# Optimization experiments

Hardware: AMD Instinct MI355X
Metric: run time of the kernel (lower is better)

## Reference

```python
import jax, jax.numpy as jnp
import numpy as np

D_MODEL = 1024
NUM_HEADS = 16
D_K = D_MODEL // NUM_HEADS


def setup_inputs() -> dict:
    key = jax.random.key(0)
    ks = jax.random.split(key, 8)
    B, S = 2, 2048
    query = jax.random.normal(ks[0], (B, S, D_MODEL), dtype=jnp.float32)
    k_in = jax.random.normal(ks[1], (B, S, D_MODEL), dtype=jnp.float32)
    value = jax.random.normal(ks[2], (B, S, D_MODEL), dtype=jnp.float32)
    # causal mask: True = masked out (upper triangle above diagonal)
    mask = jnp.triu(jnp.ones((S, S), dtype=bool), k=1)[None, None, :, :]
    scale = 1.0 / np.sqrt(D_MODEL)
    W_q = jax.random.normal(ks[3], (D_MODEL, D_MODEL), dtype=jnp.float32) * scale
    W_k = jax.random.normal(ks[4], (D_MODEL, D_MODEL), dtype=jnp.float32) * scale
    W_v = jax.random.normal(ks[5], (D_MODEL, D_MODEL), dtype=jnp.float32) * scale
    W_o = jax.random.normal(ks[6], (D_MODEL, D_MODEL), dtype=jnp.float32) * scale
    return {"query": query, "key": k_in, "value": value, "mask": mask,
            "W_q": W_q, "W_k": W_k, "W_v": W_v, "W_o": W_o}


def _split(x):
    # [B, S, d_model] -> [B, h, S, d_k]
    B, S, _ = x.shape
    return x.reshape(B, S, NUM_HEADS, D_K).transpose(0, 2, 1, 3)


def reference(query, key, value, mask, W_q, W_k, W_v, W_o):
    # torch nn.Linear(bias=False): y = x @ W.T
    Q = _split(query @ W_q.T)   # [B, h, Sq, d_k]
    K = _split(key @ W_k.T)     # [B, h, Sk, d_k]
    V = _split(value @ W_v.T)   # [B, h, Sk, d_k]
    scores = jnp.einsum('bhqd,bhkd->bhqk', Q, K) / jnp.sqrt(jnp.float32(D_K))
    scores = jnp.where(mask, -jnp.inf, scores)
    attn_w = jax.nn.softmax(scores, axis=-1)
    attn_w = jnp.nan_to_num(attn_w, nan=0.0)
    out = jnp.einsum('bhqk,bhkd->bhqd', attn_w, V)  # [B, h, Sq, d_k]
    B, _, Sq, _ = out.shape
    merged = out.transpose(0, 2, 1, 3).reshape(B, Sq, D_MODEL)
    return merged @ W_o.T
```

## Files before the change

### kernel.cpp

```cpp
#include <hip/hip_runtime.h>
#include <hip/hip_bf16.h>
#include <stdint.h>

typedef __attribute__((ext_vector_type(4))) float f32x4;
typedef __attribute__((ext_vector_type(8))) __bf16 bf16x8;
typedef __attribute__((ext_vector_type(4))) unsigned short us4;
typedef __attribute__((ext_vector_type(8))) unsigned short us8;

#define SEQ 2048
#define DMODEL 1024
#define NH 16
#define DK 64
#define MTOT 4096

__device__ __forceinline__ unsigned short f2bf(float x) {
  union { float f; unsigned int u; } v; v.f = x;
  unsigned int r = v.u + 0x7fffu + ((v.u >> 16) & 1u);
  return (unsigned short)(r >> 16);
}

__device__ __forceinline__ unsigned int cvtpk(float lo, float hi) {
  unsigned int r;
  asm("v_cvt_pk_bf16_f32 %0, %1, %2" : "=v"(r) : "v"(lo), "v"(hi));
  return r;
}

__device__ __forceinline__ f32x4 mfma_bf16(bf16x8 a, bf16x8 b, f32x4 c) {
  return __builtin_amdgcn_mfma_f32_16x16x32_bf16(a, b, c, 0, 0, 0);
}

__device__ __forceinline__ void gload16(const unsigned short* g, unsigned short* l) {
  __builtin_amdgcn_global_load_lds((__attribute__((address_space(1))) void*)g,
                                   (__attribute__((address_space(3))) void*)l,
                                   16, 0, 0);
}

__global__ void cvt_w(const float* __restrict__ s0, const float* __restrict__ s1,
                      const float* __restrict__ s2, const float* __restrict__ s3,
                      unsigned short* __restrict__ d0, unsigned short* __restrict__ d1,
                      unsigned short* __restrict__ d2, unsigned short* __restrict__ d3) {
  const int y = blockIdx.y;
  const float* s = y == 0 ? s0 : y == 1 ? s1 : y == 2 ? s2 : s3;
  unsigned short* d = y == 0 ? d0 : y == 1 ? d1 : y == 2 ? d2 : d3;
  const int n4 = DMODEL * DMODEL / 4;
  const int stride = gridDim.x * blockDim.x;
  for (int i = blockIdx.x * blockDim.x + threadIdx.x; i < n4; i += stride) {
    f32x4 v = reinterpret_cast<const f32x4*>(s)[i];
    us4 o;
    o.x = f2bf(v.x); o.y = f2bf(v.y); o.z = f2bf(v.z); o.w = f2bf(v.w);
    reinterpret_cast<us4*>(d)[i] = o;
  }
}

__global__ __launch_bounds__(256) void gemm_qk(
    const float* __restrict__ xq, const float* __restrict__ xk,
    const unsigned short* __restrict__ bwq, const unsigned short* __restrict__ bwk,
    unsigned short* __restrict__ Qh, unsigned short* __restrict__ Kh) {
  const int z = blockIdx.z;
  const float* A = z ? xk : xq;
  const unsigned short* B = z ? bwk : bwq;
  unsigned short* out = z ? Kh : Qh;
  const float scale = z ? 1.0f : 0.18033688011112042f;

  __shared__ __align__(16) unsigned short lA[128 * 32];
  __shared__ __align__(16) unsigned short lB[128 * 32];
  const int tid = threadIdx.x;
  const int lane = tid & 63;
  const int wid = tid >> 6;
  const int l15 = lane & 15, l4 = lane >> 4;
  const int bm = blockIdx.x, bn = blockIdx.y;
  const int wr = wid >> 1, wc = wid & 1;

  f32x4 acc[4][4] = {};

  const int chunk0 = (wid * 2 + 0) * 64 + lane;
  const int chunk1 = (wid * 2 + 1) * 64 + lane;
  const float* gAf0 = A + (size_t)(bm * 128 + (chunk0 >> 2)) * 1024 + (chunk0 & 3) * 8;
  const float* gAf1 = A + (size_t)(bm * 128 + (chunk1 >> 2)) * 1024 + (chunk1 & 3) * 8;
  const unsigned short* gB0 = B + (size_t)(bn * 128 + (chunk0 >> 2)) * 1024 + (chunk0 & 3) * 8;
  const unsigned short* gB1 = B + (size_t)(bn * 128 + (chunk1 >> 2)) * 1024 + (chunk1 & 3) * 8;
  unsigned short* wA0 = lA + chunk0 * 8;
  unsigned short* wA1 = lA + chunk1 * 8;
  unsigned short* lB0 = lB + (wid * 2 + 0) * 512;
  unsigned short* lB1 = lB + (wid * 2 + 1) * 512;

  f32x4 ra0 = *reinterpret_cast<const f32x4*>(gAf0);
  f32x4 ra1 = *reinterpret_cast<const f32x4*>(gAf0 + 4);
  f32x4 rb0 = *reinterpret_cast<const f32x4*>(gAf1);
  f32x4 rb1 = *reinterpret_cast<const f32x4*>(gAf1 + 4);

  for (int kt = 0; kt < 1024; kt += 32) {
    __syncthreads();
    union { us8 h; unsigned int u[4]; } p0, p1;
    p0.u[0] = cvtpk(ra0.x, ra0.y); p0.u[1] = cvtpk(ra0.z, ra0.w);
    p0.u[2] = cvtpk(ra1.x, ra1.y); p0.u[3] = cvtpk(ra1.z, ra1.w);
    p1.u[0] = cvtpk(rb0.x, rb0.y); p1.u[1] = cvtpk(rb0.z, rb0.w);
    p1.u[2] = cvtpk(rb1.x, rb1.y); p1.u[3] = cvtpk(rb1.z, rb1.w);
    *reinterpret_cast<us8*>(wA0) = p0.h;
    *reinterpret_cast<us8*>(wA1) = p1.h;
    gload16(gB0 + kt, lB0);
    gload16(gB1 + kt, lB1);
    if (kt + 32 < 1024) {
      ra0 = *reinterpret_cast<const f32x4*>(gAf0 + kt + 32);
      ra1 = *reinterpret_cast<const f32x4*>(gAf0 + kt + 36);
      rb0 = *reinterpret_cast<const f32x4*>(gAf1 + kt + 32);
      rb1 = *reinterpret_cast<const f32x4*>(gAf1 + kt + 36);
    }
    __syncthreads();
    bf16x8 af[4], bfr[4];
#pragma unroll
    for (int i = 0; i < 4; ++i)
      af[i] = *reinterpret_cast<const bf16x8*>(&lA[(wr * 64 + i * 16 + l15) * 32 + l4 * 8]);
#pragma unroll
    for (int j = 0; j < 4; ++j)
      bfr[j] = *reinterpret_cast<const bf16x8*>(&lB[(wc * 64 + j * 16 + l15) * 32 + l4 * 8]);
#pragma unroll
    for (int i = 0; i < 4; ++i)
#pragma unroll
      for (int j = 0; j < 4; ++j)
        acc[i][j] = mfma_bf16(bfr[j], af[i], acc[i][j]);
  }

  const int row0 = bm * 128 + wr * 64;
  const int col0 = bn * 128 + wc * 64;
#pragma unroll
  for (int i = 0; i < 4; ++i) {
    const int m = row0 + i * 16 + l15;
    const int b = m >> 11, s = m & 2047;
#pragma unroll
    for (int j = 0; j < 4; ++j) {
      const int n0 = col0 + j * 16 + l4 * 4;
      const int h = n0 >> 6, dd = n0 & 63;
      union { us4 h4; unsigned int u[2]; } pk;
      pk.u[0] = cvtpk(acc[i][j][0] * scale, acc[i][j][1] * scale);
      pk.u[1] = cvtpk(acc[i][j][2] * scale, acc[i][j][3] * scale);
      *reinterpret_cast<us4*>(&out[(size_t)(b * NH + h) * (SEQ * DK) + s * DK + dd]) = pk.h4;
    }
  }
}

__global__ __launch_bounds__(256) void gemm_v(
    const float* __restrict__ xv, const unsigned short* __restrict__ bwv,
    unsigned short* __restrict__ Vt) {
  __shared__ __align__(16) unsigned short lA[128 * 32];
  __shared__ __align__(16) unsigned short lB[128 * 32];
  const int tid = threadIdx.x;
  const int lane = tid & 63;
  const int wid = tid >> 6;
  const int l15 = lane & 15, l4 = lane >> 4;
  const int bm = blockIdx.x, bn = blockIdx.y;
  const int wr = wid >> 1, wc = wid & 1;

  f32x4 acc[4][4] = {};

  const int chunk0 = (wid * 2 + 0) * 64 + lane;
  const int chunk1 = (wid * 2 + 1) * 64 + lane;
  const float* gAf0 = xv + (size_t)(bm * 128 + (chunk0 >> 2)) * 1024 + (chunk0 & 3) * 8;
  const float* gAf1 = xv + (size_t)(bm * 128 + (chunk1 >> 2)) * 1024 + (chunk1 & 3) * 8;
  const unsigned short* gB0 = bwv + (size_t)(bn * 128 + (chunk0 >> 2)) * 1024 + (chunk0 & 3) * 8;
  const unsigned short* gB1 = bwv + (size_t)(bn * 128 + (chunk1 >> 2)) * 1024 + (chunk1 & 3) * 8;
  unsigned short* wA0 = lA + chunk0 * 8;
  unsigned short* wA1 = lA + chunk1 * 8;
  unsigned short* lB0 = lB + (wid * 2 + 0) * 512;
  unsigned short* lB1 = lB + (wid * 2 + 1) * 512;

  f32x4 ra0 = *reinterpret_cast<const f32x4*>(gAf0);
  f32x4 ra1 = *reinterpret_cast<const f32x4*>(gAf0 + 4);
  f32x4 rb0 = *reinterpret_cast<const f32x4*>(gAf1);
  f32x4 rb1 = *reinterpret_cast<const f32x4*>(gAf1 + 4);

  for (int kt = 0; kt < 1024; kt += 32) {
    __syncthreads();
    union { us8 h; unsigned int u[4]; } p0, p1;
    p0.u[0] = cvtpk(ra0.x, ra0.y); p0.u[1] = cvtpk(ra0.z, ra0.w);
    p0.u[2] = cvtpk(ra1.x, ra1.y); p0.u[3] = cvtpk(ra1.z, ra1.w);
    p1.u[0] = cvtpk(rb0.x, rb0.y); p1.u[1] = cvtpk(rb0.z, rb0.w);
    p1.u[2] = cvtpk(rb1.x, rb1.y); p1.u[3] = cvtpk(rb1.z, rb1.w);
    *reinterpret_cast<us8*>(wA0) = p0.h;
    *reinterpret_cast<us8*>(wA1) = p1.h;
    gload16(gB0 + kt, lB0);
    gload16(gB1 + kt, lB1);
    if (kt + 32 < 1024) {
      ra0 = *reinterpret_cast<const f32x4*>(gAf0 + kt + 32);
      ra1 = *reinterpret_cast<const f32x4*>(gAf0 + kt + 36);
      rb0 = *reinterpret_cast<const f32x4*>(gAf1 + kt + 32);
      rb1 = *reinterpret_cast<const f32x4*>(gAf1 + kt + 36);
    }
    __syncthreads();
    bf16x8 af[4], bfr[4];
#pragma unroll
    for (int i = 0; i < 4; ++i)
      af[i] = *reinterpret_cast<const bf16x8*>(&lA[(wr * 64 + i * 16 + l15) * 32 + l4 * 8]);
#pragma unroll
    for (int j = 0; j < 4; ++j)
      bfr[j] = *reinterpret_cast<const bf16x8*>(&lB[(wc * 64 + j * 16 + l15) * 32 + l4 * 8]);
#pragma unroll
    for (int i = 0; i < 4; ++i)
#pragma unroll
      for (int j = 0; j < 4; ++j)
        acc[i][j] = mfma_bf16(af[i], bfr[j], acc[i][j]);
  }

  const int row0 = bm * 128 + wr * 64;
  const int col0 = bn * 128 + wc * 64;
#pragma unroll
  for (int i = 0; i < 4; ++i) {
    const int m0 = row0 + i * 16 + l4 * 4;
    const int b = m0 >> 11, s0 = m0 & 2047;
    const int g = (s0 >> 2) & 7;
    const int col = (s0 & ~31) + ((g & 3) << 3) + ((g >> 2) << 2);
#pragma unroll
    for (int j = 0; j < 4; ++j) {
      const int n = col0 + j * 16 + l15;
      const int h = n >> 6, dd = n & 63;
      union { us4 h4; unsigned int u[2]; } pk;
      pk.u[0] = cvtpk(acc[i][j][0], acc[i][j][1]);
      pk.u[1] = cvtpk(acc[i][j][2], acc[i][j][3]);
      *reinterpret_cast<us4*>(&Vt[(size_t)(b * NH + h) * (DK * SEQ) + dd * SEQ + col]) = pk.h4;
    }
  }
}

__global__ __launch_bounds__(256) void gemm_o(const unsigned short* __restrict__ A,
                                              const unsigned short* __restrict__ B,
                                              float* __restrict__ out) {
  __shared__ __align__(16) unsigned short lA[128 * 32];
  __shared__ __align__(16) unsigned short lB[128 * 32];
  const int tid = threadIdx.x;
  const int lane = tid & 63;
  const int wid = tid >> 6;
  const int l15 = lane & 15, l4 = lane >> 4;
  const int bm = blockIdx.x, bn = blockIdx.y;
  const int wr = wid >> 1, wc = wid & 1;

  f32x4 acc[4][4] = {};

  const int chunk0 = (wid * 2 + 0) * 64 + lane;
  const int chunk1 = (wid * 2 + 1) * 64 + lane;
  const unsigned short* gA0 = A + (size_t)(bm * 128 + (chunk0 >> 2)) * 1024 + (chunk0 & 3) * 8;
  const unsigned short* gA1 = A + (size_t)(bm * 128 + (chunk1 >> 2)) * 1024 + (chunk1 & 3) * 8;
  const unsigned short* gB0 = B + (size_t)(bn * 128 + (chunk0 >> 2)) * 1024 + (chunk0 & 3) * 8;
  const unsigned short* gB1 = B + (size_t)(bn * 128 + (chunk1 >> 2)) * 1024 + (chunk1 & 3) * 8;
  unsigned short* lA0 = lA + (wid * 2 + 0) * 512;
  unsigned short* lA1 = lA + (wid * 2 + 1) * 512;
  unsigned short* lB0 = lB + (wid * 2 + 0) * 512;
  unsigned short* lB1 = lB + (wid * 2 + 1) * 512;

  for (int kt = 0; kt < 1024; kt += 32) {
    __syncthreads();
    gload16(gA0 + kt, lA0);
    gload16(gA1 + kt, lA1);
    gload16(gB0 + kt, lB0);
    gload16(gB1 + kt, lB1);
    __syncthreads();
    bf16x8 af[4], bfr[4];
#pragma unroll
    for (int i = 0; i < 4; ++i)
      af[i] = *reinterpret_cast<const bf16x8*>(&lA[(wr * 64 + i * 16 + l15) * 32 + l4 * 8]);
#pragma unroll
    for (int j = 0; j < 4; ++j)
      bfr[j] = *reinterpret_cast<const bf16x8*>(&lB[(wc * 64 + j * 16 + l15) * 32 + l4 * 8]);
#pragma unroll
    for (int i = 0; i < 4; ++i)
#pragma unroll
      for (int j = 0; j < 4; ++j)
        acc[i][j] = mfma_bf16(bfr[j], af[i], acc[i][j]);
  }

  const int row0 = bm * 128 + wr * 64;
  const int col0 = bn * 128 + wc * 64;
#pragma unroll
  for (int i = 0; i < 4; ++i) {
    const int m = row0 + i * 16 + l15;
#pragma unroll
    for (int j = 0; j < 4; ++j) {
      const int n0 = col0 + j * 16 + l4 * 4;
      *reinterpret_cast<f32x4*>(&out[(size_t)m * DMODEL + n0]) = acc[i][j];
    }
  }
}

__global__ __launch_bounds__(512, 2) void attn_kernel(const unsigned short* __restrict__ Qh,
                                                      const unsigned short* __restrict__ Kh,
                                                      const unsigned short* __restrict__ Vt,
                                                      unsigned short* __restrict__ Mg) {
  __shared__ __align__(16) unsigned short Kl[4][64 * 64];
  __shared__ __align__(16) unsigned short Vl[4][64 * 64];

  const int tid = threadIdx.x;
  const int lane = tid & 63;
  const int w = tid >> 6;
  const int l15 = lane & 15, l4 = lane >> 4;

  const int d = blockIdx.x;
  const int xcd = d & 7;
  const int j = d >> 3;
  const int bh = (j >> 3) * 8 + xcd;
  const int x = j & 7;

  const unsigned short* Qb = Qh + (size_t)bh * SEQ * DK;
  const unsigned short* Kb = Kh + (size_t)bh * SEQ * DK;
  const unsigned short* Vb = Vt + (size_t)bh * DK * SEQ;
  const int bq = bh >> 4, hh = bh & 15;
  unsigned short* Mbase = Mg + (size_t)bq * SEQ * DMODEL + hh * DK;

  const int srow = lane >> 3;
  const int sswz = (lane & 7) ^ srow;
  const unsigned short* KsrcB = Kb + (size_t)(w * 8 + srow) * DK + sswz * 8;
  const unsigned short* VsrcB = Vb + (size_t)(w * 8 + srow) * SEQ + sswz * 8;

  const int l7 = l15 & 7;

  const int taus[2] = {15 - x, x};

#pragma unroll 1
  for (int seg = 0; seg < 2; ++seg) {
    const int tau = taus[seg];
    const int qbase = tau * 128;
    const int q0w = qbase + w * 16;
    const int nt = 2 * tau + 2;

    __syncthreads();

    bf16x8 qf0 = *reinterpret_cast<const bf16x8*>(Qb + (size_t)(q0w + l15) * DK + l4 * 8);
    bf16x8 qf1 = *reinterpret_cast<const bf16x8*>(Qb + (size_t)(q0w + l15) * DK + 32 + l4 * 8);

    f32x4 o[4] = {};
    float mrow = -__builtin_inff();
    float lrow = 0.0f;

    gload16(KsrcB, &Kl[0][w * 512]);
    gload16(VsrcB, &Vl[0][w * 512]);
    gload16(KsrcB + (size_t)64 * DK, &Kl[1][w * 512]);
    gload16(VsrcB + 64, &Vl[1][w * 512]);

    const int S = nt >> 1;
#pragma unroll 1
    for (int s = 0; s < S; ++s) {
      const int t0 = s << 1;
      const int kbase0 = t0 << 6;

      asm volatile("s_waitcnt vmcnt(0)" ::: "memory");
      __builtin_amdgcn_sched_barrier(0);
      __builtin_amdgcn_s_barrier();
      __builtin_amdgcn_sched_barrier(0);

      if (t0 + 2 < nt) {
        gload16(KsrcB + (size_t)(kbase0 + 128) * DK, &Kl[(t0 + 2) & 3][w * 512]);
        gload16(VsrcB + (kbase0 + 128), &Vl[(t0 + 2) & 3][w * 512]);
        gload16(KsrcB + (size_t)(kbase0 + 192) * DK, &Kl[(t0 + 3) & 3][w * 512]);
        gload16(VsrcB + (kbase0 + 192), &Vl[(t0 + 3) & 3][w * 512]);
      }

#pragma unroll
      for (int u = 0; u < 2; ++u) {
        const int t = t0 + u;
        const int kbase = t << 6;
        if (kbase >= q0w + 16) continue;
        const unsigned short* Kc = Kl[t & 3];
        const unsigned short* Vc = Vl[t & 3];

        f32x4 sc[4];
        __builtin_amdgcn_s_setprio(1);
#pragma unroll
        for (int c = 0; c < 4; ++c) {
          const int krow = c * 16 + l15;
          bf16x8 kf0 = *reinterpret_cast<const bf16x8*>(&Kc[krow * 64 + ((l4 ^ l7) * 8)]);
          bf16x8 kf1 = *reinterpret_cast<const bf16x8*>(&Kc[krow * 64 + (((4 + l4) ^ l7) * 8)]);
          f32x4 z = {0.f, 0.f, 0.f, 0.f};
          z = mfma_bf16(kf0, qf0, z);
          sc[c] = mfma_bf16(kf1, qf1, z);
        }
        __builtin_amdgcn_s_setprio(0);

        if (kbase + 63 > q0w) {
          const int qg = q0w + l15;
#pragma unroll
          for (int c = 0; c < 4; ++c) {
            const int kp = kbase + c * 16 + l4 * 4;
#pragma unroll
            for (int r = 0; r < 4; ++r)
              if (kp + r > qg) sc[c][r] = -__builtin_inff();
          }
        }

        f32x4 mv = sc[0];
#pragma unroll
        for (int c = 1; c < 4; ++c)
#pragma unroll
          for (int r = 0; r < 4; ++r) mv[r] = fmaxf(mv[r], sc[c][r]);
        float pm = fmaxf(fmaxf(mv[0], mv[1]), fmaxf(mv[2], mv[3]));
        if (!__all(pm - mrow <= 8.0f)) {
          pm = fmaxf(pm, __shfl_xor(pm, 16));
          pm = fmaxf(pm, __shfl_xor(pm, 32));
          const float mn = fmaxf(mrow, pm);
          const float al = __builtin_amdgcn_exp2f(mrow - mn);
          mrow = mn;
          lrow *= al;
#pragma unroll
          for (int dd = 0; dd < 4; ++dd)
#pragma unroll
            for (int r = 0; r < 4; ++r) o[dd][r] *= al;
        }
        union PB { bf16x8 v; unsigned int u[4]; } pbv[2];
        f32x4 sv = {0.f, 0.f, 0.f, 0.f};
#pragma unroll
        for (int c = 0; c < 4; ++c) {
          const float p0 = __builtin_amdgcn_exp2f(sc[c][0] - mrow);
          const float p1 = __builtin_amdgcn_exp2f(sc[c][1] - mrow);
          const float p2 = __builtin_amdgcn_exp2f(sc[c][2] - mrow);
          const float p3 = __builtin_amdgcn_exp2f(sc[c][3] - mrow);
          sv[0] += p0; sv[1] += p1; sv[2] += p2; sv[3] += p3;
          pbv[c >> 1].u[(c & 1) * 2 + 0] = cvtpk(p0, p1);
          pbv[c >> 1].u[(c & 1) * 2 + 1] = cvtpk(p2, p3);
        }
        lrow += (sv[0] + sv[1]) + (sv[2] + sv[3]);

        __builtin_amdgcn_s_setprio(1);
#pragma unroll
        for (int dd = 0; dd < 4; ++dd) {
          const int vrow = dd * 16 + l15;
#pragma unroll
          for (int p = 0; p < 2; ++p) {
            const bf16x8 av = *reinterpret_cast<const bf16x8*>(
                &Vc[vrow * 64 + (((p * 4 + l4) ^ l7) * 8)]);
            o[dd] = mfma_bf16(av, pbv[p].v, o[dd]);
          }
        }
        __builtin_amdgcn_s_setprio(0);
      }
    }

    lrow += __shfl_xor(lrow, 16);
    lrow += __shfl_xor(lrow, 32);
    const float inv = __builtin_amdgcn_rcpf(lrow);
    const int s = q0w + l15;
#pragma unroll
    for (int dd = 0; dd < 4; ++dd) {
      union { us4 h; unsigned int u[2]; } pk;
      pk.u[0] = cvtpk(o[dd][0] * inv, o[dd][1] * inv);
      pk.u[1] = cvtpk(o[dd][2] * inv, o[dd][3] * inv);
      *reinterpret_cast<us4*>(&Mbase[(size_t)s * DMODEL + dd * 16 + l4 * 4]) = pk.h;
    }
  }
}

extern "C" void kernel_launch(void* const* d_in, const int* in_sizes, int n_in,
                              void* d_out, int out_size, void* d_ws, size_t ws_size,
                              hipStream_t stream) {
  (void)in_sizes; (void)n_in; (void)out_size;
  if (ws_size < (size_t)64 * (1 << 20)) return;

  const float* q = (const float*)d_in[0];
  const float* k = (const float*)d_in[1];
  const float* v = (const float*)d_in[2];
  const float* wq = (const float*)d_in[4];
  const float* wk = (const float*)d_in[5];
  const float* wv = (const float*)d_in[6];
  const float* wo = (const float*)d_in[7];

  char* ws = (char*)d_ws;
  unsigned short* bwq = (unsigned short*)(ws + (size_t)24 * (1 << 20));
  unsigned short* bwk = (unsigned short*)(ws + (size_t)26 * (1 << 20));
  unsigned short* bwv = (unsigned short*)(ws + (size_t)28 * (1 << 20));
  unsigned short* bwo = (unsigned short*)(ws + (size_t)30 * (1 << 20));
  unsigned short* Qh  = (unsigned short*)(ws + (size_t)32 * (1 << 20));
  unsigned short* Kh  = (unsigned short*)(ws + (size_t)40 * (1 << 20));
  unsigned short* Vt  = (unsigned short*)(ws + (size_t)48 * (1 << 20));
  unsigned short* Mg  = (unsigned short*)(ws + (size_t)56 * (1 << 20));

  cvt_w<<<dim3(64, 4), 256, 0, stream>>>(wq, wk, wv, wo, bwq, bwk, bwv, bwo);
  gemm_qk<<<dim3(32, 8, 2), 256, 0, stream>>>(q, k, bwq, bwk, Qh, Kh);
  gemm_v<<<dim3(32, 8), 256, 0, stream>>>(v, bwv, Vt);
  attn_kernel<<<dim3(256), 512, 0, stream>>>(Qh, Kh, Vt, Mg);
  gemm_o<<<dim3(32, 8), 256, 0, stream>>>(Mg, bwo, (float*)d_out);
}
```

Before: 127.3 us.

## Swizzle LDS in projection GEMMs and triple-buffer output GEMM

The QK and V projection GEMMs now XOR-swizzle their LDS tile layout so fragment reads avoid bank conflicts. The next fp32 A prefetch is moved after the barrier. The output GEMM is rebuilt around 512 threads, a K-tile of 64 and a three-stage async global-to-LDS ring with explicit vmcnt waits, so loads overlap the MFMA work. The cost is more LDS per block (about 96 KB), which may limit occupancy, plus more complex wait and sync logic.

```diff
diff --git a/kernel.cpp b/kernel.cpp
--- a/kernel.cpp
+++ b/kernel.cpp
@@ -75,12 +75,14 @@
 
   const int chunk0 = (wid * 2 + 0) * 64 + lane;
   const int chunk1 = (wid * 2 + 1) * 64 + lane;
-  const float* gAf0 = A + (size_t)(bm * 128 + (chunk0 >> 2)) * 1024 + (chunk0 & 3) * 8;
-  const float* gAf1 = A + (size_t)(bm * 128 + (chunk1 >> 2)) * 1024 + (chunk1 & 3) * 8;
-  const unsigned short* gB0 = B + (size_t)(bn * 128 + (chunk0 >> 2)) * 1024 + (chunk0 & 3) * 8;
-  const unsigned short* gB1 = B + (size_t)(bn * 128 + (chunk1 >> 2)) * 1024 + (chunk1 & 3) * 8;
-  unsigned short* wA0 = lA + chunk0 * 8;
-  unsigned short* wA1 = lA + chunk1 * 8;
+  const int ar0 = chunk0 >> 2, ac0 = chunk0 & 3;
+  const int ar1 = chunk1 >> 2, ac1 = chunk1 & 3;
+  const float* gAf0 = A + (size_t)(bm * 128 + ar0) * 1024 + ac0 * 8;
+  const float* gAf1 = A + (size_t)(bm * 128 + ar1) * 1024 + ac1 * 8;
+  const unsigned short* gB0 = B + (size_t)(bn * 128 + ar0) * 1024 + (ac0 ^ (ar0 & 3)) * 8;
+  const unsigned short* gB1 = B + (size_t)(bn * 128 + ar1) * 1024 + (ac1 ^ (ar1 & 3)) * 8;
+  unsigned short* wA0 = lA + ar0 * 32 + ((ac0 ^ (ar0 & 3)) * 8);
+  unsigned short* wA1 = lA + ar1 * 32 + ((ac1 ^ (ar1 & 3)) * 8);
   unsigned short* lB0 = lB + (wid * 2 + 0) * 512;
   unsigned short* lB1 = lB + (wid * 2 + 1) * 512;
 
@@ -88,6 +90,8 @@
   f32x4 ra1 = *reinterpret_cast<const f32x4*>(gAf0 + 4);
   f32x4 rb0 = *reinterpret_cast<const f32x4*>(gAf1);
   f32x4 rb1 = *reinterpret_cast<const f32x4*>(gAf1 + 4);
+
+  const int sx = l15 & 3;
 
   for (int kt = 0; kt < 1024; kt += 32) {
     __syncthreads();
@@ -100,20 +104,24 @@
     *reinterpret_cast<us8*>(wA1) = p1.h;
     gload16(gB0 + kt, lB0);
     gload16(gB1 + kt, lB1);
+    __syncthreads();
+
     if (kt + 32 < 1024) {
       ra0 = *reinterpret_cast<const f32x4*>(gAf0 + kt + 32);
       ra1 = *reinterpret_cast<const f32x4*>(gAf0 + kt + 36);
       rb0 = *reinterpret_cast<const f32x4*>(gAf1 + kt + 32);
       rb1 = *reinterpret_cast<const f32x4*>(gAf1 + kt + 36);
     }
-    __syncthreads();
+
     bf16x8 af[4], bfr[4];
 #pragma unroll
     for (int i = 0; i < 4; ++i)
-      af[i] = *reinterpret_cast<const bf16x8*>(&lA[(wr * 64 + i * 16 + l15) * 32 + l4 * 8]);
+      af[i] = *reinterpret_cast<const bf16x8*>(
+          &lA[(wr * 64 + i * 16 + l15) * 32 + ((l4 ^ sx) * 8)]);
 #pragma unroll
     for (int j = 0; j < 4; ++j)
-      bfr[j] = *reinterpret_cast<const bf16x8*>(&lB[(wc * 64 + j * 16 + l15) * 32 + l4 * 8]);
+      bfr[j] = *reinterpret_cast<const bf16x8*>(
+          &lB[(wc * 64 + j * 16 + l15) * 32 + ((l4 ^ sx) * 8)]);
 #pragma unroll
     for (int i = 0; i < 4; ++i)
 #pragma unroll
@@ -155,12 +163,14 @@
 
   const int chunk0 = (wid * 2 + 0) * 64 + lane;
   const int chunk1 = (wid * 2 + 1) * 64 + lane;
-  const float* gAf0 = xv + (size_t)(bm * 128 + (chunk0 >> 2)) * 1024 + (chunk0 & 3) * 8;
-  const float* gAf1 = xv + (size_t)(bm * 128 + (chunk1 >> 2)) * 1024 + (chunk1 & 3) * 8;
-  const unsigned short* gB0 = bwv + (size_t)(bn * 128 + (chunk0 >> 2)) * 1024 + (chunk0 & 3) * 8;
-  const unsigned short* gB1 = bwv + (size_t)(bn * 128 + (chunk1 >> 2)) * 1024 + (chunk1 & 3) * 8;
-  unsigned short* wA0 = lA + chunk0 * 8;
-  unsigned short* wA1 = lA + chunk1 * 8;
+  const int ar0 = chunk0 >> 2, ac0 = chunk0 & 3;
+  const int ar1 = chunk1 >> 2, ac1 = chunk1 & 3;
+  const float* gAf0 = xv + (size_t)(bm * 128 + ar0) * 1024 + ac0 * 8;
+  const float* gAf1 = xv + (size_t)(bm * 128 + ar1) * 1024 + ac1 * 8;
+  const unsigned short* gB0 = bwv + (size_t)(bn * 128 + ar0) * 1024 + (ac0 ^ (ar0 & 3)) * 8;
+  const unsigned short* gB1 = bwv + (size_t)(bn * 128 + ar1) * 1024 + (ac1 ^ (ar1 & 3)) * 8;
+  unsigned short* wA0 = lA + ar0 * 32 + ((ac0 ^ (ar0 & 3)) * 8);
+  unsigned short* wA1 = lA + ar1 * 32 + ((ac1 ^ (ar1 & 3)) * 8);
   unsigned short* lB0 = lB + (wid * 2 + 0) * 512;
   unsigned short* lB1 = lB + (wid * 2 + 1) * 512;
 
@@ -168,6 +178,8 @@
   f32x4 ra1 = *reinterpret_cast<const f32x4*>(gAf0 + 4);
   f32x4 rb0 = *reinterpret_cast<const f32x4*>(gAf1);
   f32x4 rb1 = *reinterpret_cast<const f32x4*>(gAf1 + 4);
+
+  const int sx = l15 & 3;
 
   for (int kt = 0; kt < 1024; kt += 32) {
     __syncthreads();
@@ -180,20 +192,24 @@
     *reinterpret_cast<us8*>(wA1) = p1.h;
     gload16(gB0 + kt, lB0);
     gload16(gB1 + kt, lB1);
+    __syncthreads();
+
     if (kt + 32 < 1024) {
       ra0 = *reinterpret_cast<const f32x4*>(gAf0 + kt + 32);
       ra1 = *reinterpret_cast<const f32x4*>(gAf0 + kt + 36);
       rb0 = *reinterpret_cast<const f32x4*>(gAf1 + kt + 32);
       rb1 = *reinterpret_cast<const f32x4*>(gAf1 + kt + 36);
     }
-    __syncthreads();
+
     bf16x8 af[4], bfr[4];
 #pragma unroll
     for (int i = 0; i < 4; ++i)
-      af[i] = *reinterpret_cast<const bf16x8*>(&lA[(wr * 64 + i * 16 + l15) * 32 + l4 * 8]);
+      af[i] = *reinterpret_cast<const bf16x8*>(
+          &lA[(wr * 64 + i * 16 + l15) * 32 + ((l4 ^ sx) * 8)]);
 #pragma unroll
     for (int j = 0; j < 4; ++j)
-      bfr[j] = *reinterpret_cast<const bf16x8*>(&lB[(wc * 64 + j * 16 + l15) * 32 + l4 * 8]);
+      bfr[j] = *reinterpret_cast<const bf16x8*>(
+          &lB[(wc * 64 + j * 16 + l15) * 32 + ((l4 ^ sx) * 8)]);
 #pragma unroll
     for (int i = 0; i < 4; ++i)
 #pragma unroll
@@ -221,56 +237,90 @@
   }
 }
 
-__global__ __launch_bounds__(256) void gemm_o(const unsigned short* __restrict__ A,
+__global__ __launch_bounds__(512) void gemm_o(const unsigned short* __restrict__ A,
                                               const unsigned short* __restrict__ B,
                                               float* __restrict__ out) {
-  __shared__ __align__(16) unsigned short lA[128 * 32];
-  __shared__ __align__(16) unsigned short lB[128 * 32];
+  __shared__ __align__(16) unsigned short lA3[3][128 * 64];
+  __shared__ __align__(16) unsigned short lB3[3][128 * 64];
+
   const int tid = threadIdx.x;
-  const int lane = tid & 63;
-  const int wid = tid >> 6;
+  const int lane = tid & 63, wid = tid >> 6;
   const int l15 = lane & 15, l4 = lane >> 4;
   const int bm = blockIdx.x, bn = blockIdx.y;
   const int wr = wid >> 1, wc = wid & 1;
 
-  f32x4 acc[4][4] = {};
-
-  const int chunk0 = (wid * 2 + 0) * 64 + lane;
-  const int chunk1 = (wid * 2 + 1) * 64 + lane;
-  const unsigned short* gA0 = A + (size_t)(bm * 128 + (chunk0 >> 2)) * 1024 + (chunk0 & 3) * 8;
-  const unsigned short* gA1 = A + (size_t)(bm * 128 + (chunk1 >> 2)) * 1024 + (chunk1 & 3) * 8;
-  const unsigned short* gB0 = B + (size_t)(bn * 128 + (chunk0 >> 2)) * 1024 + (chunk0 & 3) * 8;
-  const unsigned short* gB1 = B + (size_t)(bn * 128 + (chunk1 >> 2)) * 1024 + (chunk1 & 3) * 8;
-  unsigned short* lA0 = lA + (wid * 2 + 0) * 512;
-  unsigned short* lA1 = lA + (wid * 2 + 1) * 512;
-  unsigned short* lB0 = lB + (wid * 2 + 0) * 512;
-  unsigned short* lB1 = lB + (wid * 2 + 1) * 512;
-
-  for (int kt = 0; kt < 1024; kt += 32) {
-    __syncthreads();
-    gload16(gA0 + kt, lA0);
-    gload16(gA1 + kt, lA1);
-    gload16(gB0 + kt, lB0);
-    gload16(gB1 + kt, lB1);
-    __syncthreads();
-    bf16x8 af[4], bfr[4];
-#pragma unroll
-    for (int i = 0; i < 4; ++i)
-      af[i] = *reinterpret_cast<const bf16x8*>(&lA[(wr * 64 + i * 16 + l15) * 32 + l4 * 8]);
-#pragma unroll
-    for (int j = 0; j < 4; ++j)
-      bfr[j] = *reinterpret_cast<const bf16x8*>(&lB[(wc * 64 + j * 16 + l15) * 32 + l4 * 8]);
-#pragma unroll
-    for (int i = 0; i < 4; ++i)
-#pragma unroll
-      for (int j = 0; j < 4; ++j)
-        acc[i][j] = mfma_bf16(bfr[j], af[i], acc[i][j]);
-  }
-
-  const int row0 = bm * 128 + wr * 64;
+  f32x4 acc[2][4] = {};
+
+  const int r8 = lane >> 3, c8 = lane & 7;
+  const unsigned short* gAs[2];
+  const unsigned short* gBs[2];
+  int dstoff[2];
+#pragma unroll
+  for (int is = 0; is < 2; ++is) {
+    const int rbase = is * 64 + wid * 8;
+    gAs[is] = A + (size_t)(bm * 128 + rbase + r8) * 1024 + (c8 ^ r8) * 8;
+    gBs[is] = B + (size_t)(bn * 128 + rbase + r8) * 1024 + (c8 ^ r8) * 8;
+    dstoff[is] = rbase * 64;
+  }
+
+#define STAGE_O(t, buf)                                         \
+  {                                                             \
+    const int kb = (t) * 64;                                    \
+    gload16(gAs[0] + kb, &lA3[buf][dstoff[0]]);                 \
+    gload16(gAs[1] + kb, &lA3[buf][dstoff[1]]);                 \
+    gload16(gBs[0] + kb, &lB3[buf][dstoff[0]]);                 \
+    gload16(gBs[1] + kb, &lB3[buf][dstoff[1]]);                 \
+  }
+
+  STAGE_O(0, 0);
+  STAGE_O(1, 1);
+
+#pragma unroll 1
+  for (int t = 0; t < 16; ++t) {
+    if (t + 1 < 16) {
+      asm volatile("s_waitcnt vmcnt(4)" ::: "memory");
+    } else {
+      asm volatile("s_waitcnt vmcnt(0)" ::: "memory");
+    }
+    __builtin_amdgcn_sched_barrier(0);
+    __builtin_amdgcn_s_barrier();
+    __builtin_amdgcn_sched_barrier(0);
+
+    if (t + 2 < 16) {
+      const int pb = (t + 2) % 3;
+      STAGE_O(t + 2, pb);
+    }
+
+    const unsigned short* La = lA3[t % 3];
+    const unsigned short* Lb = lB3[t % 3];
+#pragma unroll
+    for (int kk = 0; kk < 2; ++kk) {
+      bf16x8 af[2], bf[4];
+#pragma unroll
+      for (int i = 0; i < 2; ++i) {
+        const int row = wr * 32 + i * 16 + l15;
+        af[i] = *reinterpret_cast<const bf16x8*>(
+            &La[row * 64 + (((kk * 4 + l4) ^ (l15 & 7)) * 8)]);
+      }
+#pragma unroll
+      for (int j = 0; j < 4; ++j) {
+        const int row = wc * 64 + j * 16 + l15;
+        bf[j] = *reinterpret_cast<const bf16x8*>(
+            &Lb[row * 64 + (((kk * 4 + l4) ^ (l15 & 7)) * 8)]);
+      }
+#pragma unroll
+      for (int i = 0; i < 2; ++i)
+#pragma unroll
+        for (int j = 0; j < 4; ++j)
+          acc[i][j] = mfma_bf16(bf[j], af[i], acc[i][j]);
+    }
+  }
+#undef STAGE_O
+
+  const int row0 = bm * 128 + wr * 32;
   const int col0 = bn * 128 + wc * 64;
 #pragma unroll
-  for (int i = 0; i < 4; ++i) {
+  for (int i = 0; i < 2; ++i) {
     const int m = row0 + i * 16 + l15;
 #pragma unroll
     for (int j = 0; j < 4; ++j) {
@@ -473,5 +523,5 @@
   gemm_qk<<<dim3(32, 8, 2), 256, 0, stream>>>(q, k, bwq, bwk, Qh, Kh);
   gemm_v<<<dim3(32, 8), 256, 0, stream>>>(v, bwv, Vt);
   attn_kernel<<<dim3(256), 512, 0, stream>>>(Qh, Kh, Vt, Mg);
-  gemm_o<<<dim3(32, 8), 256, 0, stream>>>(Mg, bwo, (float*)d_out);
-}
+  gemm_o<<<dim3(32, 8), 512, 0, stream>>>(Mg, bwo, (float*)d_out);
+}
```

Measured after the change: 122.8 us. 3.5% less time.
